# Kernel tuning notes

Hardware: AMD Instinct MI355X
Metric: run time of the kernel (lower is better)

The kernel has to match this reference:

```python
import jax, jax.numpy as jnp
import numpy as np

I = 1024  # input_size
H = 1024  # hidden_size


def setup_inputs() -> dict:
    key = jax.random.key(0)
    ks = jax.random.split(key, 13)
    s_i = 1.0 / np.sqrt(I)
    s_h = 1.0 / np.sqrt(H)
    x = jax.random.normal(ks[0], (64, 512, I), dtype=jnp.float32)
    # nn.Linear weights are [out, in]; biases only on the U (recurrent) linears.
    Wi = jax.random.uniform(ks[1], (H, I), jnp.float32, -s_i, s_i)
    Wf = jax.random.uniform(ks[2], (H, I), jnp.float32, -s_i, s_i)
    Wo = jax.random.uniform(ks[3], (H, I), jnp.float32, -s_i, s_i)
    Wg = jax.random.uniform(ks[4], (H, I), jnp.float32, -s_i, s_i)
    Ui = jax.random.uniform(ks[5], (H, H), jnp.float32, -s_h, s_h)
    Uf = jax.random.uniform(ks[6], (H, H), jnp.float32, -s_h, s_h)
    Uo = jax.random.uniform(ks[7], (H, H), jnp.float32, -s_h, s_h)
    Ug = jax.random.uniform(ks[8], (H, H), jnp.float32, -s_h, s_h)
    bi = jax.random.uniform(ks[9], (H,), jnp.float32, -s_h, s_h)
    bf = jax.random.uniform(ks[10], (H,), jnp.float32, -s_h, s_h)
    bo = jax.random.uniform(ks[11], (H,), jnp.float32, -s_h, s_h)
    bg = jax.random.uniform(ks[12], (H,), jnp.float32, -s_h, s_h)
    return {"x": x, "Wi": Wi, "Wf": Wf, "Wo": Wo, "Wg": Wg,
            "Ui": Ui, "Uf": Uf, "Uo": Uo, "Ug": Ug,
            "bi": bi, "bf": bf, "bo": bo, "bg": bg}


def reference(x, Wi, Wf, Wo, Wg, Ui, Uf, Uo, Ug, bi, bf, bo, bg):
    B, T, _ = x.shape
    Hdim = Ui.shape[0]
    # Precompute all input-to-gate projections in one batched contraction: [T, B, H] each.
    Wcat = jnp.concatenate([Wi, Wf, Wo, Wg], axis=0)          # [4H, I]
    xg = jnp.einsum('bti,gi->tbg', x, Wcat)                   # [T, B, 4H]
    xi, xf, xo, xgt = jnp.split(xg, 4, axis=-1)

    h0 = jnp.zeros((B, Hdim), x.dtype)
    c0 = jnp.zeros((B, Hdim), x.dtype)

    def step(carry, gates_t):
        h, c = carry
        gi, gf, go, gg = gates_t
        i = jax.nn.sigmoid(gi + h @ Ui.T + bi)
        f = jax.nn.sigmoid(gf + h @ Uf.T + bf)
        o = jax.nn.sigmoid(go + h @ Uo.T + bo)
        g = jnp.tanh(gg + h @ Ug.T + bg)
        c = f * c + i * g
        h = o * jnp.tanh(c)
        return (h, c), h

    (h_last, c_last), hs = jax.lax.scan(step, (h0, c0), (xi, xf, xo, xgt))
    return jnp.transpose(hs, (1, 0, 2)), h_last, c_last  # [B, T, H], [B, H], [B, H]
```

## Files before the change

kernel.cpp:

```cpp
#include <hip/hip_runtime.h>
#include <stdint.h>
#include <stddef.h>


typedef unsigned short u16;
typedef unsigned int u32;
typedef short bf16x8 __attribute__((ext_vector_type(8)));
typedef float f32x4 __attribute__((ext_vector_type(4)));
typedef u32 u32x4 __attribute__((ext_vector_type(4)));

#define B_ 64
#define T_ 512
#define I_ 1024
#define H_ 1024
#define NWG 64
#define BTH (B_ * T_ * H_)

#define OFF_XB 0UL
#define OFF_WT 67108864UL
#define OFF_UT 75497472UL
#define OFF_XG 83886080UL
#define OFF_HB 352321536UL
#define OFF_FLG 352583680UL

#define EPOCH_MASK 0x40004000u
#define EPOCH_CLR  0xBFFFBFFFu

__device__ __forceinline__ u16 f2bf(float f) {
  u32 u = __builtin_bit_cast(u32, f);
  return (u16)((u + 0x7FFFu + ((u >> 16) & 1u)) >> 16);
}
__device__ __forceinline__ float bf2f(u16 h) {
  u32 u = ((u32)h) << 16;
  return __builtin_bit_cast(float, u);
}
__device__ __forceinline__ float sigm(float x) { return 1.f / (1.f + __expf(-x)); }
__device__ __forceinline__ float tanh_(float x) {
  float e = __expf(-2.f * fabsf(x));
  float t = (1.f - e) / (1.f + e);
  return x >= 0.f ? t : -t;
}
__device__ __forceinline__ void async16(const void* g, void* l) {
  __builtin_amdgcn_global_load_lds((const __attribute__((address_space(1))) void*)g,
                                   (__attribute__((address_space(3))) void*)l, 16, 0, 0);
}
__device__ __forceinline__ void st_u32_sc1(u32* p, u32 v) {
  asm volatile("global_store_dword %0, %1, off sc1" : : "v"(p), "v"(v) : "memory");
}
__device__ __forceinline__ u32x4 ld16_sc1(const u16* p) {
  u32x4 r;
  asm volatile("global_load_dwordx4 %0, %1, off sc1" : "=v"(r) : "v"(p) : "memory");
  return r;
}

__global__ void k_init(u16* hbuf, u32* flg) {
  int i = blockIdx.x * 256 + threadIdx.x;
  uint4 z;
  if (i < 8192) {
    z.x = 0u; z.y = 0u; z.z = 0u; z.w = 0u;
  } else {
    z.x = EPOCH_MASK; z.y = EPOCH_MASK; z.z = EPOCH_MASK; z.w = EPOCH_MASK;
  }
  ((uint4*)hbuf)[i] = z;
  if (i < NWG) flg[i] = 0u;
}

__global__ void k_cvt_x(const float4* __restrict__ x, ushort4* __restrict__ xb) {
  size_t i = (size_t)blockIdx.x * 256 + threadIdx.x;
  float4 v = x[i];
  ushort4 o;
  o.x = f2bf(v.x); o.y = f2bf(v.y); o.z = f2bf(v.z); o.w = f2bf(v.w);
  xb[i] = o;
}

__global__ void k_cvt_w(const float* __restrict__ Wi, const float* __restrict__ Wf,
                        const float* __restrict__ Wo, const float* __restrict__ Wg,
                        const float* __restrict__ Ui, const float* __restrict__ Uf,
                        const float* __restrict__ Uo, const float* __restrict__ Ug,
                        u16* __restrict__ Wt, u16* __restrict__ Ut) {
  int idx = blockIdx.x * 256 + threadIdx.x;
  int r = idx >> 7;
  int s = idx & 127;
  int w = r >> 6, c = r & 63, g = c >> 4, jl = c & 15;
  int hrow = w * 16 + jl;
  const float* Wsrc = (g == 0) ? Wi : (g == 1) ? Wf : (g == 2) ? Wo : Wg;
  const float* Usrc = (g == 0) ? Ui : (g == 1) ? Uf : (g == 2) ? Uo : Ug;
  int so = hrow * 1024 + s * 8;
  int dovr = r * 1024 + s * 8;
  ushort4 a, b;
  a.x = f2bf(Wsrc[so + 0]); a.y = f2bf(Wsrc[so + 1]); a.z = f2bf(Wsrc[so + 2]); a.w = f2bf(Wsrc[so + 3]);
  b.x = f2bf(Wsrc[so + 4]); b.y = f2bf(Wsrc[so + 5]); b.z = f2bf(Wsrc[so + 6]); b.w = f2bf(Wsrc[so + 7]);
  *(ushort4*)&Wt[dovr] = a;
  *(ushort4*)&Wt[dovr + 4] = b;
  a.x = f2bf(Usrc[so + 0]); a.y = f2bf(Usrc[so + 1]); a.z = f2bf(Usrc[so + 2]); a.w = f2bf(Usrc[so + 3]);
  b.x = f2bf(Usrc[so + 4]); b.y = f2bf(Usrc[so + 5]); b.z = f2bf(Usrc[so + 6]); b.w = f2bf(Usrc[so + 7]);
  *(ushort4*)&Ut[dovr] = a;
  *(ushort4*)&Ut[dovr + 4] = b;
}

__global__ __launch_bounds__(256) void k_gemm(const u16* __restrict__ xb,
                                              const u16* __restrict__ Wt,
                                              u16* __restrict__ xg) {
  __shared__ u16 As[4 * 128 * 8];
  __shared__ u16 Bs[4 * 128 * 8];
  const int tid = threadIdx.x;
  const int lane = tid & 63, wave = tid >> 6;
  const int wm = wave >> 1, wn = wave & 1;
  const int lr = lane & 15, lq = lane >> 4;
  const int m0 = blockIdx.y * 128, n0 = blockIdx.x * 128;

  f32x4 acc[4][4];
#pragma unroll
  for (int mt = 0; mt < 4; ++mt)
#pragma unroll
    for (int nt = 0; nt < 4; ++nt) acc[mt][nt] = {0.f, 0.f, 0.f, 0.f};

  for (int kk = 0; kk < 32; ++kk) {
    int k0 = kk * 32;
    __syncthreads();
#pragma unroll
    for (int uu = 0; uu < 2; ++uu) {
      int u = wave * 2 + uu;
      int kq = u >> 1, rh = u & 1;
      int row = rh * 64 + lane;
      async16(&xb[(size_t)(m0 + row) * 1024 + k0 + kq * 8], &As[kq * 1024 + rh * 512]);
      async16(&Wt[(size_t)(n0 + row) * 1024 + k0 + kq * 8], &Bs[kq * 1024 + rh * 512]);
    }
    __syncthreads();

    bf16x8 af[4], bfr[4];
#pragma unroll
    for (int mt = 0; mt < 4; ++mt)
      af[mt] = *(const bf16x8*)&As[lq * 1024 + (wm * 64 + mt * 16 + lr) * 8];
#pragma unroll
    for (int nt = 0; nt < 4; ++nt)
      bfr[nt] = *(const bf16x8*)&Bs[lq * 1024 + (wn * 64 + nt * 16 + lr) * 8];
#pragma unroll
    for (int mt = 0; mt < 4; ++mt)
#pragma unroll
      for (int nt = 0; nt < 4; ++nt)
        acc[mt][nt] = __builtin_amdgcn_mfma_f32_16x16x32_bf16(af[mt], bfr[nt], acc[mt][nt], 0, 0, 0);
  }

#pragma unroll
  for (int mt = 0; mt < 4; ++mt)
#pragma unroll
    for (int nt = 0; nt < 4; ++nt)
#pragma unroll
      for (int r = 0; r < 4; ++r) {
        int mg = m0 + wm * 64 + mt * 16 + lq * 4 + r;
        int ngl = n0 + wn * 64 + nt * 16 + lr;
        int b = mg >> 9, t = mg & 511;
        int w = ngl >> 6, c = ngl & 63;
        xg[(size_t)t * 262144 + w * 4096 + b * 64 + c] = f2bf(acc[mt][nt][r]);
      }
}

__global__ __launch_bounds__(512, 2) void k_lstm(
    const u16* __restrict__ Ut, const u16* __restrict__ xg, u16* hbuf,
    const float* __restrict__ bi, const float* __restrict__ bf_,
    const float* __restrict__ bo, const float* __restrict__ bg,
    float* __restrict__ out) {
  __shared__ __align__(16) unsigned char LDSB[131072];
  u16* hL = (u16*)LDSB;
  float* P = (float*)LDSB;

  const int tid = threadIdx.x;
  const int lane = tid & 63, wave = tid >> 6;
  const int lr = lane & 15, lq = lane >> 4;
  const int kq = wave >> 1, ng = wave & 1;
  const int w = blockIdx.x;

  bf16x8 Bf[2][8];
#pragma unroll
  for (int nt = 0; nt < 2; ++nt)
#pragma unroll
    for (int ks = 0; ks < 8; ++ks) {
      int n = w * 64 + ng * 32 + nt * 16 + lr;
      int k = kq * 256 + ks * 32 + lq * 8;
      Bf[nt][ks] = *(const bf16x8*)&Ut[(size_t)n * 1024 + k];
    }

  const int q = wave, b = lane;
  float bia[2][4];
#pragma unroll
  for (int p = 0; p < 2; ++p) {
    int hc = w * 16 + q * 2 + p;
    bia[p][0] = bi[hc]; bia[p][1] = bf_[hc]; bia[p][2] = bo[hc]; bia[p][3] = bg[hc];
  }
  float cst0 = 0.f, cst1 = 0.f;
  const int Gh = w * 2 + (q >> 2);
  const int c8 = (q * 2) & 7;

  for (int t = 0; t < T_; ++t) {
    const u16* hin = hbuf + (size_t)(t & 1) * 65536;
    const u32 em = ((t >> 1) & 1) ? EPOCH_MASK : 0u;

    const u16* xgp = xg + (size_t)t * 262144 + w * 4096;
    u32 xv[4];
#pragma unroll
    for (int g = 0; g < 4; ++g)
      xv[g] = *(const u32*)&xgp[b * 64 + g * 16 + q * 2];

    {
      u32x4 v[16];
      u32 pend = 0xFFFFu;
      int spin = 0;
      do {
        if (spin > 1) __builtin_amdgcn_s_sleep(1);
        ++spin;
#pragma unroll
        for (int i = 0; i < 16; ++i)
          if (pend & (1u << i))
            v[i] = ld16_sc1(hin + (size_t)(tid + (i << 9)) * 8);
        asm volatile("s_waitcnt vmcnt(0)"
                     : "+v"(v[0]), "+v"(v[1]), "+v"(v[2]), "+v"(v[3]),
                       "+v"(v[4]), "+v"(v[5]), "+v"(v[6]), "+v"(v[7]),
                       "+v"(v[8]), "+v"(v[9]), "+v"(v[10]), "+v"(v[11]),
                       "+v"(v[12]), "+v"(v[13]), "+v"(v[14]), "+v"(v[15])
                     :: "memory");
        __builtin_amdgcn_sched_barrier(0);
#pragma unroll
        for (int i = 0; i < 16; ++i)
          if (pend & (1u << i)) {
            u32 d = ((v[i][0] ^ em) | (v[i][1] ^ em) | (v[i][2] ^ em) | (v[i][3] ^ em))
                    & EPOCH_MASK;
            if (d == 0u) {
              u32x4 wv;
              wv[0] = v[i][0] & EPOCH_CLR;
              wv[1] = v[i][1] & EPOCH_CLR;
              wv[2] = v[i][2] & EPOCH_CLR;
              wv[3] = v[i][3] & EPOCH_CLR;
              *(u32x4*)&hL[(size_t)(tid + (i << 9)) * 8] = wv;
              pend &= ~(1u << i);
            }
          }
      } while (pend);
    }
    __syncthreads();

    f32x4 acc[4][2];
#pragma unroll
    for (int mt = 0; mt < 4; ++mt) { acc[mt][0] = {0.f,0.f,0.f,0.f}; acc[mt][1] = {0.f,0.f,0.f,0.f}; }

#pragma unroll
    for (int ks = 0; ks < 8; ++ks) {
      int Gk = kq * 32 + ks * 4 + lq;
      bf16x8 af[4];
#pragma unroll
      for (int mt = 0; mt < 4; ++mt)
        af[mt] = *(const bf16x8*)&hL[(Gk * 64 + mt * 16 + lr) * 8];
#pragma unroll
      for (int mt = 0; mt < 4; ++mt) {
        acc[mt][0] = __builtin_amdgcn_mfma_f32_16x16x32_bf16(af[mt], Bf[0][ks], acc[mt][0], 0, 0, 0);
        acc[mt][1] = __builtin_amdgcn_mfma_f32_16x16x32_bf16(af[mt], Bf[1][ks], acc[mt][1], 0, 0, 0);
      }
    }
    __syncthreads();

#pragma unroll
    for (int mt = 0; mt < 4; ++mt)
#pragma unroll
      for (int nt = 0; nt < 2; ++nt)
#pragma unroll
        for (int r = 0; r < 4; ++r) {
          int m = mt * 16 + lq * 4 + r;
          int cc = nt * 16 + lr;
          P[((ng * 4 + kq) * 64 + m) * 34 + cc] = acc[mt][nt][r];
        }
    __syncthreads();

    float hv[2];
#pragma unroll
    for (int p = 0; p < 2; ++p) {
      int jl = q * 2 + p;
      float pre[4];
#pragma unroll
      for (int g = 0; g < 4; ++g) {
        int cc = (g & 1) * 16 + jl;
        int base = (g >> 1) * 4 * 64;
        float s = P[(base + 0 * 64 + b) * 34 + cc] + P[(base + 1 * 64 + b) * 34 + cc] +
                  P[(base + 2 * 64 + b) * 34 + cc] + P[(base + 3 * 64 + b) * 34 + cc];
        u16 xh = (u16)(p == 0 ? (xv[g] & 0xFFFFu) : (xv[g] >> 16));
        pre[g] = s + bf2f(xh) + bia[p][g];
      }
      float iv = sigm(pre[0]);
      float fv = sigm(pre[1]);
      float ov = sigm(pre[2]);
      float gv = tanh_(pre[3]);
      float cn = fv * (p == 0 ? cst0 : cst1) + iv * gv;
      if (p == 0) cst0 = cn; else cst1 = cn;
      hv[p] = ov * tanh_(cn);
    }

    float2 f2v; f2v.x = hv[0]; f2v.y = hv[1];
    if (t < T_ - 1) {
      u16* hout = hbuf + (size_t)((t + 1) & 1) * 65536;
      u32 hpack = (u32)f2bf(hv[0]) | ((u32)f2bf(hv[1]) << 16);
      if (((t + 1) >> 1) & 1) hpack |= EPOCH_MASK;
      st_u32_sc1((u32*)&hout[(size_t)(Gh * 64 + b) * 8 + c8], hpack);
      *(float2*)&out[((size_t)b * 512 + t) * 1024 + w * 16 + q * 2] = f2v;
    } else {
      *(float2*)&out[((size_t)b * 512 + t) * 1024 + w * 16 + q * 2] = f2v;
      *(float2*)&out[(size_t)BTH + b * 1024 + w * 16 + q * 2] = f2v;
      float2 c2v; c2v.x = cst0; c2v.y = cst1;
      *(float2*)&out[(size_t)BTH + B_ * H_ + b * 1024 + w * 16 + q * 2] = c2v;
    }
    __syncthreads();
  }
}

extern "C" void kernel_launch(void* const* d_in, const int* in_sizes, int n_in,
                              void* d_out, int out_size, void* d_ws, size_t ws_size,
                              hipStream_t stream) {
  const float* x  = (const float*)d_in[0];
  const float* Wi = (const float*)d_in[1];
  const float* Wf = (const float*)d_in[2];
  const float* Wo = (const float*)d_in[3];
  const float* Wg = (const float*)d_in[4];
  const float* Ui = (const float*)d_in[5];
  const float* Uf = (const float*)d_in[6];
  const float* Uo = (const float*)d_in[7];
  const float* Ug = (const float*)d_in[8];
  const float* bi = (const float*)d_in[9];
  const float* bf = (const float*)d_in[10];
  const float* bo = (const float*)d_in[11];
  const float* bg = (const float*)d_in[12];
  float* out = (float*)d_out;

  char* ws = (char*)d_ws;
  u16* xb   = (u16*)(ws + OFF_XB);
  u16* Wt   = (u16*)(ws + OFF_WT);
  u16* Ut   = (u16*)(ws + OFF_UT);
  u16* xg   = (u16*)(ws + OFF_XG);
  u16* hbuf = (u16*)(ws + OFF_HB);
  u32* flg  = (u32*)(ws + OFF_FLG);

  k_init<<<64, 256, 0, stream>>>(hbuf, flg);
  k_cvt_x<<<32768, 256, 0, stream>>>((const float4*)x, (ushort4*)xb);
  k_cvt_w<<<2048, 256, 0, stream>>>(Wi, Wf, Wo, Wg, Ui, Uf, Uo, Ug, Wt, Ut);
  k_gemm<<<dim3(32, 256), 256, 0, stream>>>(xb, Wt, xg);
  k_lstm<<<NWG, 512, 0, stream>>>(Ut, xg, hbuf, bi, bf, bo, bg, out);
}
```

Before: 4.488 ms.

## Replace block barriers with per-wave-pair LDS counters and coalesce h stores

Each pair of waves now loads and polls only the slice of h that its own MFMA K-quarter consumes. Pairs synchronise through an LDS atomic counter instead of a full __syncthreads, so a pair can start its matmul as soon as its own data arrives. The h output is staged in LDS and written as 16-byte stores by two waves instead of scattered 4-byte stores, and the epoch check is split into branch-specific AND/OR tests. The trailing barrier is removed, which relies on the new intra-step barrier and the pair counters for correctness when LDS regions are reused across steps. That adds some risk of races.

```diff
diff --git a/kernel.cpp b/kernel.cpp
--- a/kernel.cpp
+++ b/kernel.cpp
@@ -26,6 +26,10 @@
 #define EPOCH_MASK 0x40004000u
 #define EPOCH_CLR  0xBFFFBFFFu
 
+#define LDS_HX 131072
+#define LDS_QC 133120
+#define LDS_SZ 133184
+
 __device__ __forceinline__ u16 f2bf(float f) {
   u32 u = __builtin_bit_cast(u32, f);
   return (u16)((u + 0x7FFFu + ((u >> 16) & 1u)) >> 16);
@@ -44,13 +48,13 @@
   __builtin_amdgcn_global_load_lds((const __attribute__((address_space(1))) void*)g,
                                    (__attribute__((address_space(3))) void*)l, 16, 0, 0);
 }
-__device__ __forceinline__ void st_u32_sc1(u32* p, u32 v) {
-  asm volatile("global_store_dword %0, %1, off sc1" : : "v"(p), "v"(v) : "memory");
-}
 __device__ __forceinline__ u32x4 ld16_sc1(const u16* p) {
   u32x4 r;
   asm volatile("global_load_dwordx4 %0, %1, off sc1" : "=v"(r) : "v"(p) : "memory");
   return r;
+}
+__device__ __forceinline__ void st16_sc1(u16* p, u32x4 v) {
+  asm volatile("global_store_dwordx4 %0, %1, off sc1" : : "v"(p), "v"(v) : "memory");
 }
 
 __global__ void k_init(u16* hbuf, u32* flg) {
@@ -161,15 +165,20 @@
     const float* __restrict__ bi, const float* __restrict__ bf_,
     const float* __restrict__ bo, const float* __restrict__ bg,
     float* __restrict__ out) {
-  __shared__ __align__(16) unsigned char LDSB[131072];
+  __shared__ __align__(16) unsigned char LDSB[LDS_SZ];
   u16* hL = (u16*)LDSB;
   float* P = (float*)LDSB;
+  u32* hX = (u32*)(LDSB + LDS_HX);
+  u32* qc = (u32*)(LDSB + LDS_QC);
 
   const int tid = threadIdx.x;
   const int lane = tid & 63, wave = tid >> 6;
   const int lr = lane & 15, lq = lane >> 4;
   const int kq = wave >> 1, ng = wave & 1;
+  const int pairtid = ng * 64 + lane;
   const int w = blockIdx.x;
+
+  if (tid < 4) qc[tid] = 0u;
 
   bf16x8 Bf[2][8];
 #pragma unroll
@@ -189,12 +198,12 @@
     bia[p][0] = bi[hc]; bia[p][1] = bf_[hc]; bia[p][2] = bo[hc]; bia[p][3] = bg[hc];
   }
   float cst0 = 0.f, cst1 = 0.f;
-  const int Gh = w * 2 + (q >> 2);
-  const int c8 = (q * 2) & 7;
+
+  __syncthreads();
 
   for (int t = 0; t < T_; ++t) {
     const u16* hin = hbuf + (size_t)(t & 1) * 65536;
-    const u32 em = ((t >> 1) & 1) ? EPOCH_MASK : 0u;
+    const int ep = (t >> 1) & 1;
 
     const u16* xgp = xg + (size_t)t * 262144 + w * 4096;
     u32 xv[4];
@@ -212,7 +221,7 @@
 #pragma unroll
         for (int i = 0; i < 16; ++i)
           if (pend & (1u << i))
-            v[i] = ld16_sc1(hin + (size_t)(tid + (i << 9)) * 8);
+            v[i] = ld16_sc1(hin + (size_t)(kq * 2048 + pairtid + (i << 7)) * 8);
         asm volatile("s_waitcnt vmcnt(0)"
                      : "+v"(v[0]), "+v"(v[1]), "+v"(v[2]), "+v"(v[3]),
                        "+v"(v[4]), "+v"(v[5]), "+v"(v[6]), "+v"(v[7]),
@@ -220,24 +229,41 @@
                        "+v"(v[12]), "+v"(v[13]), "+v"(v[14]), "+v"(v[15])
                      :: "memory");
         __builtin_amdgcn_sched_barrier(0);
-#pragma unroll
-        for (int i = 0; i < 16; ++i)
-          if (pend & (1u << i)) {
-            u32 d = ((v[i][0] ^ em) | (v[i][1] ^ em) | (v[i][2] ^ em) | (v[i][3] ^ em))
-                    & EPOCH_MASK;
-            if (d == 0u) {
-              u32x4 wv;
-              wv[0] = v[i][0] & EPOCH_CLR;
-              wv[1] = v[i][1] & EPOCH_CLR;
-              wv[2] = v[i][2] & EPOCH_CLR;
-              wv[3] = v[i][3] & EPOCH_CLR;
-              *(u32x4*)&hL[(size_t)(tid + (i << 9)) * 8] = wv;
-              pend &= ~(1u << i);
+        if (ep) {
+#pragma unroll
+          for (int i = 0; i < 16; ++i)
+            if (pend & (1u << i)) {
+              u32 aa = v[i][0] & v[i][1] & v[i][2] & v[i][3];
+              if ((aa & EPOCH_MASK) == EPOCH_MASK) {
+                u32x4 wv;
+                wv[0] = v[i][0] & EPOCH_CLR; wv[1] = v[i][1] & EPOCH_CLR;
+                wv[2] = v[i][2] & EPOCH_CLR; wv[3] = v[i][3] & EPOCH_CLR;
+                *(u32x4*)&hL[(size_t)(kq * 2048 + pairtid + (i << 7)) * 8] = wv;
+                pend &= ~(1u << i);
+              }
             }
-          }
+        } else {
+#pragma unroll
+          for (int i = 0; i < 16; ++i)
+            if (pend & (1u << i)) {
+              u32 oo = v[i][0] | v[i][1] | v[i][2] | v[i][3];
+              if ((oo & EPOCH_MASK) == 0u) {
+                *(u32x4*)&hL[(size_t)(kq * 2048 + pairtid + (i << 7)) * 8] = v[i];
+                pend &= ~(1u << i);
+              }
+            }
+        }
       } while (pend);
     }
-    __syncthreads();
+    asm volatile("s_waitcnt lgkmcnt(0)" ::: "memory");
+    if (lane == 0) atomicAdd(&qc[kq], 1u);
+    {
+      volatile u32* qp = (volatile u32*)&qc[kq];
+      u32 tgt = 2u * (u32)(t + 1);
+      while (*qp < tgt) {}
+    }
+    __builtin_amdgcn_sched_barrier(0);
+    asm volatile("" ::: "memory");
 
     f32x4 acc[4][2];
 #pragma unroll
@@ -294,19 +320,25 @@
     }
 
     float2 f2v; f2v.x = hv[0]; f2v.y = hv[1];
+    *(float2*)&out[((size_t)b * 512 + t) * 1024 + w * 16 + q * 2] = f2v;
+
     if (t < T_ - 1) {
-      u16* hout = hbuf + (size_t)((t + 1) & 1) * 65536;
       u32 hpack = (u32)f2bf(hv[0]) | ((u32)f2bf(hv[1]) << 16);
       if (((t + 1) >> 1) & 1) hpack |= EPOCH_MASK;
-      st_u32_sc1((u32*)&hout[(size_t)(Gh * 64 + b) * 8 + c8], hpack);
-      *(float2*)&out[((size_t)b * 512 + t) * 1024 + w * 16 + q * 2] = f2v;
+      hX[b * 8 + q] = hpack;
+      __syncthreads();
+      if ((wave == 0) | (wave == 2)) {
+        int gg = wave >> 1;
+        u32x4 hv4 = *(const u32x4*)&hX[lane * 8 + gg * 4];
+        u16* dst = hbuf + (size_t)((t + 1) & 1) * 65536 +
+                   (size_t)((2 * w + gg) * 64 + lane) * 8;
+        st16_sc1(dst, hv4);
+      }
     } else {
-      *(float2*)&out[((size_t)b * 512 + t) * 1024 + w * 16 + q * 2] = f2v;
       *(float2*)&out[(size_t)BTH + b * 1024 + w * 16 + q * 2] = f2v;
       float2 c2v; c2v.x = cst0; c2v.y = cst1;
       *(float2*)&out[(size_t)BTH + B_ * H_ + b * 1024 + w * 16 + q * 2] = c2v;
     }
-    __syncthreads();
   }
 }
 
```

Measured after the change: 3.936 ms. 1.14x faster.
